# Kernel tuning notes

Hardware: AMD Instinct MI355X
Metric: run time of the kernel (lower is better)

The kernel has to match this reference:

```python
import jax, jax.numpy as jnp
import numpy as np

NEG_SLOPE = 0.2
BN_EPS = 1e-5


def gat_conv(x, W_src, W_dst, att_src, att_dst, bias, src, dst, num_nodes):
    # PyG GATConv, heads=1, concat=True, self-loops already included in (src,dst)
    h_src = x @ W_src                      # [N, H]
    h_dst = x @ W_dst                      # [N, H]
    a_src = h_src @ att_src                # [N]
    a_dst = h_dst @ att_dst                # [N]
    e = jax.nn.leaky_relu(a_src[src] + a_dst[dst], NEG_SLOPE)   # [E]
    # segment softmax over incoming edges of each dst node
    m = jax.ops.segment_max(e, dst, num_segments=num_nodes)     # [N]
    p = jnp.exp(e - m[dst])
    denom = jax.ops.segment_sum(p, dst, num_segments=num_nodes) # [N]
    alpha = p / denom[dst]                                      # [E]
    msgs = alpha[:, None] * h_src[src]                           # [E, H]
    out = jax.ops.segment_sum(msgs, dst, num_segments=num_nodes)
    return out + bias


def setup_inputs() -> dict:
    key = jax.random.key(0)
    ks = jax.random.split(key, 20)
    N, D_IN, H1, H2, FC, C = 100000, 256, 128, 128, 64, 40
    E = 1600000
    inp = {}
    inp['x'] = jax.random.normal(ks[0], (N, D_IN), dtype=jnp.float32)
    inp['edge_index'] = jax.random.randint(ks[1], (2, E), 0, N, dtype=jnp.int64)
    s = 1.0 / np.sqrt(D_IN)
    inp['W1_src'] = jax.random.uniform(ks[2], (D_IN, H1), jnp.float32, -s, s)
    inp['W1_dst'] = jax.random.uniform(ks[3], (D_IN, H1), jnp.float32, -s, s)
    inp['att1_src'] = jax.random.normal(ks[4], (H1,), jnp.float32) * 0.1
    inp['att1_dst'] = jax.random.normal(ks[5], (H1,), jnp.float32) * 0.1
    inp['b1'] = jnp.zeros((H1,), jnp.float32)
    s = 1.0 / np.sqrt(H1)
    inp['W2_src'] = jax.random.uniform(ks[6], (H1, H2), jnp.float32, -s, s)
    inp['W2_dst'] = jax.random.uniform(ks[7], (H1, H2), jnp.float32, -s, s)
    inp['att2_src'] = jax.random.normal(ks[8], (H2,), jnp.float32) * 0.1
    inp['att2_dst'] = jax.random.normal(ks[9], (H2,), jnp.float32) * 0.1
    inp['b2'] = jnp.zeros((H2,), jnp.float32)
    s = 1.0 / np.sqrt(H2)
    inp['fc1_w'] = jax.random.uniform(ks[10], (H2, FC), jnp.float32, -s, s)
    inp['fc1_b'] = jax.random.uniform(ks[11], (FC,), jnp.float32, -s, s)
    inp['gamma'] = jnp.ones((FC,), jnp.float32)
    inp['beta'] = jnp.zeros((FC,), jnp.float32)
    s = 1.0 / np.sqrt(FC)
    inp['fc2_w'] = jax.random.uniform(ks[12], (FC, C), jnp.float32, -s, s)
    inp['fc2_b'] = jax.random.uniform(ks[13], (C,), jnp.float32, -s, s)
    return inp


def reference(x, edge_index, W1_src, W1_dst, att1_src, att1_dst, b1,
              W2_src, W2_dst, att2_src, att2_dst, b2,
              fc1_w, fc1_b, gamma, beta, fc2_w, fc2_b):
    N = x.shape[0]
    loops = jnp.arange(N, dtype=edge_index.dtype)
    src = jnp.concatenate([edge_index[0], loops])
    dst = jnp.concatenate([edge_index[1], loops])
    h = jax.nn.relu(gat_conv(x, W1_src, W1_dst, att1_src, att1_dst, b1, src, dst, N))
    h = jax.nn.relu(gat_conv(h, W2_src, W2_dst, att2_src, att2_dst, b2, src, dst, N))
    h = h @ fc1_w + fc1_b                   # [N, 64]
    mu = jnp.mean(h, axis=0)
    var = jnp.var(h, axis=0)
    h = (h - mu) * jax.lax.rsqrt(var + BN_EPS) * gamma + beta
    h = jax.nn.relu(h)
    h = h @ fc2_w + fc2_b                   # [N, C]
    return jax.nn.log_softmax(h, axis=-1)
```

## Files before the change

### kernel.cpp

```cpp
#include <hip/hip_runtime.h>
#include <cstddef>

#define LSLOPE 0.2f
#define BN_EPS 1e-5f

__device__ __forceinline__ float lrelu(float x) { return x > 0.f ? x : LSLOPE * x; }

using half4 = __attribute__((ext_vector_type(4))) _Float16;
using half8 = __attribute__((ext_vector_type(8))) _Float16;
using f32x4 = __attribute__((ext_vector_type(4))) float;

struct h2 { _Float16 h, l; };
__device__ __forceinline__ h2 split2h(float x) {
  h2 r;
  r.h = (_Float16)x;
  r.l = (_Float16)(x - (float)r.h);
  return r;
}

__device__ __forceinline__ unsigned short f2bf(float x) {
  unsigned u = __float_as_uint(x);
  unsigned r = (u + 0x7fffu + ((u >> 16) & 1u)) >> 16;
  return (unsigned short)r;
}
__device__ __forceinline__ float bflo(unsigned int u) { return __uint_as_float(u << 16); }
__device__ __forceinline__ float bfhi(unsigned int u) { return __uint_as_float(u & 0xffff0000u); }

__device__ __forceinline__ void bfrag_body(const float* __restrict__ B, _Float16* __restrict__ bh,
                                           _Float16* __restrict__ bl, int K, int M, int t) {
  int KB = K >> 5;
  int lane = t & 63;
  int ckb  = t >> 6;
  int c  = ckb / KB, kb = ckb % KB;
  int mr = lane & 15, quad = lane >> 4;
  int col = c * 16 + mr;
  size_t obase = (size_t)t * 8;
#pragma unroll
  for (int j = 0; j < 8; ++j) {
    int k = kb * 32 + quad * 8 + j;
    h2 s = split2h(B[(size_t)k * M + col]);
    bh[obase + j] = s.h;
    bl[obase + j] = s.l;
  }
}

__device__ __forceinline__ void matvec_body(const float* __restrict__ A, const float* __restrict__ v,
                                            float* __restrict__ out, int R, int K, int t) {
  int w = t >> 6;
  int lane = t & 63;
  if (w >= R) return;
  const float* row = A + (size_t)w * K;
  float s = 0.f;
  for (int k = lane; k < K; k += 64) s = fmaf(row[k], v[k], s);
#pragma unroll
  for (int off = 32; off; off >>= 1) s += __shfl_xor(s, off, 64);
  if (lane == 0) out[w] = s;
}

__global__ __launch_bounds__(256) void prep_k(const float* __restrict__ W1s, const float* __restrict__ W2s,
                                              const float* __restrict__ fc1w,
                                              const float* __restrict__ W1d, const float* __restrict__ att1d,
                                              const float* __restrict__ W2d, const float* __restrict__ att2d,
                                              _Float16* B1h, _Float16* B1l, _Float16* B2h, _Float16* B2l,
                                              _Float16* Bfh, _Float16* Bfl,
                                              float* wvd1, float* wvd2) {
  int b = blockIdx.x;
  int tid = threadIdx.x;
  if (b < 16)       bfrag_body(W1s, B1h, B1l, 256, 128, b * 256 + tid);
  else if (b < 24)  bfrag_body(W2s, B2h, B2l, 128, 128, (b - 16) * 256 + tid);
  else if (b < 28)  bfrag_body(fc1w, Bfh, Bfl, 128, 64, (b - 24) * 256 + tid);
  else if (b < 92)  matvec_body(W1d, att1d, wvd1, 256, 128, (b - 28) * 256 + tid);
  else              matvec_body(W2d, att2d, wvd2, 128, 128, (b - 92) * 256 + tid);
}

template<int MCOLS>
__global__ __launch_bounds__(256) void gemm3h_k(const float* __restrict__ A,
                                                const _Float16* __restrict__ Bh,
                                                const _Float16* __restrict__ Bl,
                                                float* __restrict__ Cf,
                                                unsigned short* __restrict__ Cbf,
                                                const float* __restrict__ attv,
                                                float* __restrict__ asrc,
                                                const float* __restrict__ wvd,
                                                float* __restrict__ adout,
                                                int N, int K,
                                                const float* __restrict__ bias) {
  constexpr int CT = MCOLS / 16;
  __shared__ __align__(16) _Float16 sAh[2][128 * 32];
  __shared__ __align__(16) _Float16 sAl[2][128 * 32];
  const int tid  = threadIdx.x;
  const int row0 = blockIdx.x * 128;
  const int wv   = tid >> 6;
  const int lane = tid & 63;
  const int quad = lane >> 4;
  const int mr   = lane & 15;
  const int KB   = K >> 5;

  int srow[4], skc[4], soff[4];
  bool sok[4];
#pragma unroll
  for (int cc = 0; cc < 4; ++cc) {
    int s = tid + cc * 256;
    srow[cc] = s >> 3;
    skc[cc]  = (s & 7) << 2;
    soff[cc] = srow[cc] * 32 + ((skc[cc] + srow[cc] * 8) & 31);
    sok[cc]  = (row0 + srow[cc]) < N;
  }

  f32x4 acc[2][CT];
#pragma unroll
  for (int r = 0; r < 2; ++r)
#pragma unroll
    for (int c = 0; c < CT; ++c) acc[r][c] = (f32x4){0.f, 0.f, 0.f, 0.f};
  float pad[2] = {0.f, 0.f};

  float4 pf[4];
#pragma unroll
  for (int cc = 0; cc < 4; ++cc)
    pf[cc] = sok[cc] ? *(const float4*)&A[(size_t)(row0 + srow[cc]) * K + skc[cc]]
                     : make_float4(0.f, 0.f, 0.f, 0.f);
#pragma unroll
  for (int cc = 0; cc < 4; ++cc) {
    h2 s0 = split2h(pf[cc].x), s1 = split2h(pf[cc].y), s2 = split2h(pf[cc].z), s3 = split2h(pf[cc].w);
    half4 h4, l4;
    h4[0] = s0.h; h4[1] = s1.h; h4[2] = s2.h; h4[3] = s3.h;
    l4[0] = s0.l; l4[1] = s1.l; l4[2] = s2.l; l4[3] = s3.l;
    *(half4*)&sAh[0][soff[cc]] = h4;
    *(half4*)&sAl[0][soff[cc]] = l4;
  }
  __syncthreads();

  for (int kb = 0; kb < KB; ++kb) {
    const int cur = kb & 1, nxt = cur ^ 1;
    const int kk = kb << 5;
    if (kb + 1 < KB) {
      const int kn = (kb + 1) << 5;
#pragma unroll
      for (int cc = 0; cc < 4; ++cc)
        pf[cc] = sok[cc] ? *(const float4*)&A[(size_t)(row0 + srow[cc]) * K + kn + skc[cc]]
                         : make_float4(0.f, 0.f, 0.f, 0.f);
    }

    half8 ah[2], al[2];
#pragma unroll
    for (int r = 0; r < 2; ++r) {
      int row = wv * 32 + r * 16 + mr;
      int off = row * 32 + ((quad + row) & 3) * 8;
      ah[r] = *(const half8*)&sAh[cur][off];
      al[r] = *(const half8*)&sAl[cur][off];
    }
    if (wvd) {
      const float* wp = wvd + kk + quad * 8;
#pragma unroll
      for (int r = 0; r < 2; ++r) {
        float d = 0.f;
#pragma unroll
        for (int j = 0; j < 8; ++j) {
          float av = wp[j];
          d = fmaf((float)ah[r][j], av, d);
          d = fmaf((float)al[r][j], av, d);
        }
        pad[r] += d;
      }
    }
    const _Float16* bb_h = Bh + ((size_t)kb * 64 + lane) * 8;
    const _Float16* bb_l = Bl + ((size_t)kb * 64 + lane) * 8;
    const size_t cstride = (size_t)KB * 512;
#pragma unroll
    for (int c0 = 0; c0 < CT; c0 += 4) {
      half8 bh4[4], bl4[4];
#pragma unroll
      for (int c = 0; c < 4; ++c) {
        size_t o = (size_t)(c0 + c) * cstride;
        bh4[c] = *(const half8*)&bb_h[o];
        bl4[c] = *(const half8*)&bb_l[o];
      }
#pragma unroll
      for (int r = 0; r < 2; ++r)
#pragma unroll
        for (int c = 0; c < 4; ++c) {
          f32x4 a = acc[r][c0 + c];
          a = __builtin_amdgcn_mfma_f32_16x16x32_f16(al[r], bh4[c], a, 0, 0, 0);
          a = __builtin_amdgcn_mfma_f32_16x16x32_f16(ah[r], bl4[c], a, 0, 0, 0);
          a = __builtin_amdgcn_mfma_f32_16x16x32_f16(ah[r], bh4[c], a, 0, 0, 0);
          acc[r][c0 + c] = a;
        }
    }
    if (kb + 1 < KB) {
#pragma unroll
      for (int cc = 0; cc < 4; ++cc) {
        h2 s0 = split2h(pf[cc].x), s1 = split2h(pf[cc].y), s2 = split2h(pf[cc].z), s3 = split2h(pf[cc].w);
        half4 h4, l4;
        h4[0] = s0.h; h4[1] = s1.h; h4[2] = s2.h; h4[3] = s3.h;
        l4[0] = s0.l; l4[1] = s1.l; l4[2] = s2.l; l4[3] = s3.l;
        *(half4*)&sAh[nxt][soff[cc]] = h4;
        *(half4*)&sAl[nxt][soff[cc]] = l4;
      }
    }
    __syncthreads();
  }

  float pa[2][4];
#pragma unroll
  for (int r = 0; r < 2; ++r)
#pragma unroll
    for (int q = 0; q < 4; ++q) pa[r][q] = 0.f;

#pragma unroll
  for (int r = 0; r < 2; ++r)
#pragma unroll
    for (int c = 0; c < CT; ++c) {
      float av = attv ? attv[c * 16 + mr] : 0.f;
#pragma unroll
      for (int q = 0; q < 4; ++q) {
        int grow = row0 + wv * 32 + r * 16 + quad * 4 + q;
        float val = acc[r][c][q];
        if (bias) val += bias[c * 16 + mr];
        if (grow < N) {
          int gcol = c * 16 + mr;
          if (Cf)  Cf[(size_t)grow * MCOLS + gcol] = val;
          if (Cbf) Cbf[(size_t)grow * 128 + gcol] = f2bf(val);
        }
        if (attv) pa[r][q] = fmaf(val, av, pa[r][q]);
      }
    }
  if (attv) {
#pragma unroll
    for (int r = 0; r < 2; ++r)
#pragma unroll
      for (int q = 0; q < 4; ++q) {
        float p2 = pa[r][q];
        p2 += __shfl_xor(p2, 1, 64);
        p2 += __shfl_xor(p2, 2, 64);
        p2 += __shfl_xor(p2, 4, 64);
        p2 += __shfl_xor(p2, 8, 64);
        int grow = row0 + wv * 32 + r * 16 + quad * 4 + q;
        if (mr == 0 && grow < N) asrc[grow] = p2;
      }
  }
  if (wvd) {
#pragma unroll
    for (int r = 0; r < 2; ++r) {
      float d = pad[r];
      d += __shfl_xor(d, 16, 64);
      d += __shfl_xor(d, 32, 64);
      int grow = row0 + wv * 32 + r * 16 + mr;
      if (quad == 0 && grow < N) adout[grow] = d;
    }
  }
}

template<int MCOLS>
__global__ __launch_bounds__(256) void gemm3p_k(const _Float16* __restrict__ Ah,
                                                const _Float16* __restrict__ Al,
                                                const _Float16* __restrict__ Bh,
                                                const _Float16* __restrict__ Bl,
                                                float* __restrict__ Cf,
                                                unsigned short* __restrict__ Cbf,
                                                const float* __restrict__ attv,
                                                float* __restrict__ asrc,
                                                int N, int K,
                                                const float* __restrict__ bias) {
  constexpr int CT = MCOLS / 16;
  __shared__ __align__(16) _Float16 sAh[2][128 * 32];
  __shared__ __align__(16) _Float16 sAl[2][128 * 32];
  const int tid  = threadIdx.x;
  const int row0 = blockIdx.x * 128;
  const int wv   = tid >> 6;
  const int lane = tid & 63;
  const int quad = lane >> 4;
  const int mr   = lane & 15;
  const int KB   = K >> 5;

  int srow[2], sk8[2], soff[2];
  bool sok[2];
#pragma unroll
  for (int cc = 0; cc < 2; ++cc) {
    int s = tid + cc * 256;
    srow[cc] = s >> 2;
    sk8[cc]  = (s & 3) << 3;
    soff[cc] = srow[cc] * 32 + ((sk8[cc] + srow[cc] * 8) & 31);
    sok[cc]  = (row0 + srow[cc]) < N;
  }

  f32x4 acc[2][CT];
#pragma unroll
  for (int r = 0; r < 2; ++r)
#pragma unroll
    for (int c = 0; c < CT; ++c) acc[r][c] = (f32x4){0.f, 0.f, 0.f, 0.f};

  uint4 ph[2], pl[2];
  const uint4 z4 = make_uint4(0u, 0u, 0u, 0u);
#pragma unroll
  for (int cc = 0; cc < 2; ++cc) {
    size_t go = (size_t)(row0 + srow[cc]) * K + sk8[cc];
    ph[cc] = sok[cc] ? *(const uint4*)&Ah[go] : z4;
    pl[cc] = sok[cc] ? *(const uint4*)&Al[go] : z4;
  }
#pragma unroll
  for (int cc = 0; cc < 2; ++cc) {
    *(uint4*)&sAh[0][soff[cc]] = ph[cc];
    *(uint4*)&sAl[0][soff[cc]] = pl[cc];
  }
  __syncthreads();

  for (int kb = 0; kb < KB; ++kb) {
    const int cur = kb & 1, nxt = cur ^ 1;
    if (kb + 1 < KB) {
      const int kk = (kb + 1) << 5;
#pragma unroll
      for (int cc = 0; cc < 2; ++cc) {
        size_t go = (size_t)(row0 + srow[cc]) * K + kk + sk8[cc];
        ph[cc] = sok[cc] ? *(const uint4*)&Ah[go] : z4;
        pl[cc] = sok[cc] ? *(const uint4*)&Al[go] : z4;
      }
    }

    half8 ah[2], al[2];
#pragma unroll
    for (int r = 0; r < 2; ++r) {
      int row = wv * 32 + r * 16 + mr;
      int off = row * 32 + ((quad + row) & 3) * 8;
      ah[r] = *(const half8*)&sAh[cur][off];
      al[r] = *(const half8*)&sAl[cur][off];
    }
    const _Float16* bb_h = Bh + ((size_t)kb * 64 + lane) * 8;
    const _Float16* bb_l = Bl + ((size_t)kb * 64 + lane) * 8;
    const size_t cstride = (size_t)KB * 512;
#pragma unroll
    for (int c0 = 0; c0 < CT; c0 += 4) {
      half8 bh4[4], bl4[4];
#pragma unroll
      for (int c = 0; c < 4; ++c) {
        size_t o = (size_t)(c0 + c) * cstride;
        bh4[c] = *(const half8*)&bb_h[o];
        bl4[c] = *(const half8*)&bb_l[o];
      }
#pragma unroll
      for (int r = 0; r < 2; ++r)
#pragma unroll
        for (int c = 0; c < 4; ++c) {
          f32x4 a = acc[r][c0 + c];
          a = __builtin_amdgcn_mfma_f32_16x16x32_f16(al[r], bh4[c], a, 0, 0, 0);
          a = __builtin_amdgcn_mfma_f32_16x16x32_f16(ah[r], bl4[c], a, 0, 0, 0);
          a = __builtin_amdgcn_mfma_f32_16x16x32_f16(ah[r], bh4[c], a, 0, 0, 0);
          acc[r][c0 + c] = a;
        }
    }
    if (kb + 1 < KB) {
#pragma unroll
      for (int cc = 0; cc < 2; ++cc) {
        *(uint4*)&sAh[nxt][soff[cc]] = ph[cc];
        *(uint4*)&sAl[nxt][soff[cc]] = pl[cc];
      }
    }
    __syncthreads();
  }

  float pa[2][4];
#pragma unroll
  for (int r = 0; r < 2; ++r)
#pragma unroll
    for (int q = 0; q < 4; ++q) pa[r][q] = 0.f;

#pragma unroll
  for (int r = 0; r < 2; ++r)
#pragma unroll
    for (int c = 0; c < CT; ++c) {
      float av = attv ? attv[c * 16 + mr] : 0.f;
#pragma unroll
      for (int q = 0; q < 4; ++q) {
        int grow = row0 + wv * 32 + r * 16 + quad * 4 + q;
        float val = acc[r][c][q];
        if (bias) val += bias[c * 16 + mr];
        if (grow < N) {
          int gcol = c * 16 + mr;
          if (Cf)  Cf[(size_t)grow * MCOLS + gcol] = val;
          if (Cbf) Cbf[(size_t)grow * 128 + gcol] = f2bf(val);
        }
        if (attv) pa[r][q] = fmaf(val, av, pa[r][q]);
      }
    }
  if (attv) {
#pragma unroll
    for (int r = 0; r < 2; ++r)
#pragma unroll
      for (int q = 0; q < 4; ++q) {
        float p2 = pa[r][q];
        p2 += __shfl_xor(p2, 1, 64);
        p2 += __shfl_xor(p2, 2, 64);
        p2 += __shfl_xor(p2, 4, 64);
        p2 += __shfl_xor(p2, 8, 64);
        int grow = row0 + wv * 32 + r * 16 + quad * 4 + q;
        if (mr == 0 && grow < N) asrc[grow] = p2;
      }
  }
}

__global__ void deg_count_k(const int* __restrict__ edst, int E, int N, int* __restrict__ deg) {
  int i = blockIdx.x * 256 + threadIdx.x;
  if (i >= E + N) return;
  int d = (i < E) ? edst[i] : (i - E);
  atomicAdd(&deg[d], 1);
}

__global__ __launch_bounds__(1024) void scan1_k(const int* __restrict__ deg, int n,
                                                int* __restrict__ ex, int* __restrict__ bsum) {
  __shared__ int sm[1024];
  int t = threadIdx.x;
  int idx = blockIdx.x * 1024 + t;
  int v = (idx < n) ? deg[idx] : 0;
  sm[t] = v;
  __syncthreads();
  for (int off = 1; off < 1024; off <<= 1) {
    int tv = (t >= off) ? sm[t - off] : 0;
    __syncthreads();
    sm[t] += tv;
    __syncthreads();
  }
  if (idx < n) ex[idx] = sm[t] - v;
  if (t == 1023) bsum[blockIdx.x] = sm[t];
}

__global__ void scan3_k(int* __restrict__ ex, const int* __restrict__ bsum, int n, int nb, int total,
                        int* __restrict__ cursor) {
  __shared__ int pbase[2];
  int idx = blockIdx.x * 256 + threadIdx.x;
  int bin0 = (blockIdx.x * 256) >> 10;
  if (threadIdx.x < 2) {
    int b = bin0 + threadIdx.x;
    int s = 0;
    for (int i = 0; i < b && i < nb; ++i) s += bsum[i];
    pbase[threadIdx.x] = s;
  }
  __syncthreads();
  if (idx < n) {
    int v = ex[idx] + pbase[(idx >> 10) - bin0];
    ex[idx] = v;
    cursor[idx] = v;
  }
  if (idx == 0) ex[n] = total;
}

__global__ void scatter_range_k(const int* __restrict__ esrc, const int* __restrict__ edst,
                                int E, int N, int d0, int d1,
                                int* __restrict__ cursor, int* __restrict__ csr_src) {
  int i = blockIdx.x * 256 + threadIdx.x;
  if (i >= E + N) return;
  int d = (i < E) ? edst[i] : (i - E);
  if (d < d0 || d >= d1) return;
  int s = (i < E) ? esrc[i] : d;
  int pos = atomicAdd(&cursor[d], 1);
  csr_src[pos] = s;
}

__global__ __launch_bounds__(256) void gat_agg_k(const unsigned short* __restrict__ hbf,
                                                 const float* __restrict__ a_src,
                                                 const float* __restrict__ a_dst, const int* __restrict__ rowstart,
                                                 const int* __restrict__ csr_src, const float* __restrict__ bias,
                                                 _Float16* __restrict__ oh, _Float16* __restrict__ ol,
                                                 const float* __restrict__ wvd, float* __restrict__ ad_out,
                                                 int N) {
  int w = (blockIdx.x * blockDim.x + threadIdx.x) >> 6;
  int lane = threadIdx.x & 63;
  if (w >= N) return;
  int s0 = rowstart[w];
  int s1 = rowstart[w + 1];
  int deg = s1 - s0;
  float ad = a_dst[w];

  int sA = 0;
  float eA = -3.0e38f;
  if (lane < deg) {
    sA = csr_src[s0 + lane];
    eA = lrelu(a_src[sA] + ad);
  }
  float m = eA;
  for (int j = s0 + 64 + lane; j < s1; j += 64) {
    int s = csr_src[j];
    m = fmaxf(m, lrelu(a_src[s] + ad));
  }
#pragma unroll
  for (int off = 32; off; off >>= 1) m = fmaxf(m, __shfl_xor(m, off, 64));

  float preg = (lane < deg) ? __expf(eA - m) : 0.f;
  float den = preg;
  for (int j = s0 + 64 + lane; j < s1; j += 64) {
    int s = csr_src[j];
    den += __expf(lrelu(a_src[s] + ad) - m);
  }
#pragma unroll
  for (int off = 32; off; off >>= 1) den += __shfl_xor(den, off, 64);
  float inv = 1.f / den;

  const int q  = lane >> 4;
  const int sl = lane & 15;
  const uint4* hrow4 = (const uint4*)hbf;
  float acc[8];
#pragma unroll
  for (int i = 0; i < 8; ++i) acc[i] = 0.f;

  int lim  = deg < 64 ? deg : 64;
  int lim4 = (lim + 3) & ~3;
  for (int jj = 0; jj < lim4; jj += 4) {
    int e = jj + q;
    int s = __shfl(sA, e, 64);
    float wgt = __shfl(preg, e, 64) * inv;
    uint4 u = hrow4[(size_t)s * 16 + sl];
    acc[0] = fmaf(wgt, bflo(u.x), acc[0]);
    acc[1] = fmaf(wgt, bfhi(u.x), acc[1]);
    acc[2] = fmaf(wgt, bflo(u.y), acc[2]);
    acc[3] = fmaf(wgt, bfhi(u.y), acc[3]);
    acc[4] = fmaf(wgt, bflo(u.z), acc[4]);
    acc[5] = fmaf(wgt, bfhi(u.z), acc[5]);
    acc[6] = fmaf(wgt, bflo(u.w), acc[6]);
    acc[7] = fmaf(wgt, bfhi(u.w), acc[7]);
  }
  for (int j = s0 + 64 + q; j < s1; j += 4) {
    int s = csr_src[j];
    float wgt = __expf(lrelu(a_src[s] + ad) - m) * inv;
    uint4 u = hrow4[(size_t)s * 16 + sl];
    acc[0] = fmaf(wgt, bflo(u.x), acc[0]);
    acc[1] = fmaf(wgt, bfhi(u.x), acc[1]);
    acc[2] = fmaf(wgt, bflo(u.y), acc[2]);
    acc[3] = fmaf(wgt, bfhi(u.y), acc[3]);
    acc[4] = fmaf(wgt, bflo(u.z), acc[4]);
    acc[5] = fmaf(wgt, bfhi(u.z), acc[5]);
    acc[6] = fmaf(wgt, bflo(u.w), acc[6]);
    acc[7] = fmaf(wgt, bfhi(u.w), acc[7]);
  }
#pragma unroll
  for (int i = 0; i < 8; ++i) {
    acc[i] += __shfl_xor(acc[i], 16, 64);
    acc[i] += __shfl_xor(acc[i], 32, 64);
  }
  if (q == 0) {
    float4 b0 = *(const float4*)&bias[8 * sl];
    float4 b1 = *(const float4*)&bias[8 * sl + 4];
    float v[8];
    v[0] = fmaxf(acc[0] + b0.x, 0.f);
    v[1] = fmaxf(acc[1] + b0.y, 0.f);
    v[2] = fmaxf(acc[2] + b0.z, 0.f);
    v[3] = fmaxf(acc[3] + b0.w, 0.f);
    v[4] = fmaxf(acc[4] + b1.x, 0.f);
    v[5] = fmaxf(acc[5] + b1.y, 0.f);
    v[6] = fmaxf(acc[6] + b1.z, 0.f);
    v[7] = fmaxf(acc[7] + b1.w, 0.f);
    half8 vh, vl;
#pragma unroll
    for (int i = 0; i < 8; ++i) {
      h2 s = split2h(v[i]);
      vh[i] = s.h;
      vl[i] = s.l;
    }
    size_t base = (size_t)w * 128 + 8 * sl;
    *(half8*)&oh[base] = vh;
    *(half8*)&ol[base] = vl;
    if (wvd) {
      float4 w0 = *(const float4*)&wvd[8 * sl];
      float4 w1 = *(const float4*)&wvd[8 * sl + 4];
      float dd = v[0] * w0.x + v[1] * w0.y + v[2] * w0.z + v[3] * w0.w
               + v[4] * w1.x + v[5] * w1.y + v[6] * w1.z + v[7] * w1.w;
      dd += __shfl_xor(dd, 1, 64);
      dd += __shfl_xor(dd, 2, 64);
      dd += __shfl_xor(dd, 4, 64);
      dd += __shfl_xor(dd, 8, 64);
      if (sl == 0) ad_out[w] = dd;
    }
  }
}

__global__ __launch_bounds__(256) void bn_stats_k(const float* __restrict__ z, int N,
                                                  float* __restrict__ sums, float* __restrict__ sumsq) {
  __shared__ float ls[256], lq[256];
  int col = threadIdx.x & 63;
  int rg = threadIdx.x >> 6;
  float s = 0.f, q = 0.f;
  for (int r = blockIdx.x * 4 + rg; r < N; r += gridDim.x * 4) {
    float v = z[(size_t)r * 64 + col];
    s += v;
    q = fmaf(v, v, q);
  }
  ls[threadIdx.x] = s;
  lq[threadIdx.x] = q;
  __syncthreads();
  if (threadIdx.x < 64) {
    s = ls[col] + ls[col + 64] + ls[col + 128] + ls[col + 192];
    q = lq[col] + lq[col + 64] + lq[col + 128] + lq[col + 192];
    atomicAdd(&sums[col], s);
    atomicAdd(&sumsq[col], q);
  }
}

__global__ __launch_bounds__(256) void fc2_lsm_k(const float* __restrict__ z,
                                                 const float* __restrict__ sums, const float* __restrict__ sumsq,
                                                 const float* __restrict__ gamma, const float* __restrict__ beta,
                                                 const float* __restrict__ w,
                                                 const float* __restrict__ b, float* __restrict__ out,
                                                 int N, float invN) {
  __shared__ float ssc[64], ssh[64];
  if (threadIdx.x < 64) {
    int c = threadIdx.x;
    float mean = sums[c] * invN;
    float var = sumsq[c] * invN - mean * mean;
    float rs = rsqrtf(var + BN_EPS);
    float sc = gamma[c] * rs;
    ssc[c] = sc;
    ssh[c] = beta[c] - mean * sc;
  }
  __syncthreads();
  int n = blockIdx.x * 256 + threadIdx.x;
  if (n >= N) return;
  float o[40];
#pragma unroll
  for (int c = 0; c < 40; ++c) o[c] = b[c];
  const float* zr = z + (size_t)n * 64;
  for (int k = 0; k < 64; ++k) {
    float v = fmaxf(fmaf(zr[k], ssc[k], ssh[k]), 0.f);
#pragma unroll
    for (int c = 0; c < 40; ++c) o[c] = fmaf(v, w[k * 40 + c], o[c]);
  }
  float mx = o[0];
#pragma unroll
  for (int c = 1; c < 40; ++c) mx = fmaxf(mx, o[c]);
  float s = 0.f;
#pragma unroll
  for (int c = 0; c < 40; ++c) s += __expf(o[c] - mx);
  float ls = __logf(s);
  float* orow = out + (size_t)n * 40;
#pragma unroll
  for (int c = 0; c < 40; ++c) orow[c] = o[c] - mx - ls;
}

static inline char* al16(char* p) { return (char*)(((size_t)p + 15) & ~(size_t)15); }

extern "C" void kernel_launch(void* const* d_in, const int* in_sizes, int n_in,
                              void* d_out, int out_size, void* d_ws, size_t ws_size,
                              hipStream_t stream) {
  const float* x     = (const float*)d_in[0];
  const int*   eidx  = (const int*)d_in[1];
  const float* W1s   = (const float*)d_in[2];
  const float* W1d   = (const float*)d_in[3];
  const float* att1s = (const float*)d_in[4];
  const float* att1d = (const float*)d_in[5];
  const float* b1    = (const float*)d_in[6];
  const float* W2s   = (const float*)d_in[7];
  const float* W2d   = (const float*)d_in[8];
  const float* att2s = (const float*)d_in[9];
  const float* att2d = (const float*)d_in[10];
  const float* b2    = (const float*)d_in[11];
  const float* fc1w  = (const float*)d_in[12];
  const float* fc1b  = (const float*)d_in[13];
  const float* gamma = (const float*)d_in[14];
  const float* beta  = (const float*)d_in[15];
  const float* fc2w  = (const float*)d_in[16];
  const float* fc2b  = (const float*)d_in[17];
  float* out = (float*)d_out;

  const int N  = in_sizes[0] / 256;
  const int E  = in_sizes[1] / 2;
  const int ET = E + N;
  const int DIN = 256, H1 = 128;

  char* p = (char*)d_ws;
  int* deg      = (int*)p;     p += (size_t)N * 4;
  float* sums   = (float*)p;   p += 64 * 4;
  float* sumsq  = (float*)p;   p += 64 * 4;
  unsigned short* bhA = (unsigned short*)p; p += (size_t)N * 128 * 2;
  _Float16* hAh = (_Float16*)p;  p += (size_t)N * 128 * 2;
  _Float16* hAl = (_Float16*)p;  p += (size_t)N * 128 * 2;
  float* hF = (float*)p;         p += (size_t)N * 64 * 4;
  int* rowstart = (int*)p;     p += (size_t)(N + 1) * 4;
  int* cursor   = (int*)p;     p += (size_t)N * 4;
  int* csr_src  = (int*)p;     p += (size_t)ET * 4;
  float* a_src  = (float*)p;   p += (size_t)N * 4;
  float* a_dst  = (float*)p;   p += (size_t)N * 4;
  float* a_dst2 = (float*)p;   p += (size_t)N * 4;
  float* wvd1   = (float*)p;   p += 256 * 4;
  float* wvd2   = (float*)p;   p += 128 * 4;
  int* bsum     = (int*)p;     p += 256 * 4;
  p = al16(p);
  _Float16* B1h = (_Float16*)p; p += (size_t)256 * 128 * 2;
  _Float16* B1l = (_Float16*)p; p += (size_t)256 * 128 * 2;
  _Float16* B2h = (_Float16*)p; p += (size_t)128 * 128 * 2;
  _Float16* B2l = (_Float16*)p; p += (size_t)128 * 128 * 2;
  _Float16* Bfh = (_Float16*)p; p += (size_t)128 * 64 * 2;
  _Float16* Bfl = (_Float16*)p; p += (size_t)128 * 64 * 2;

  const int* esrc = eidx;
  const int* edst = eidx + E;

  hipMemsetAsync(deg, 0, (size_t)N * 4 + 512, stream);

  deg_count_k<<<(ET + 255) / 256, 256, 0, stream>>>(edst, E, N, deg);
  int nb = (N + 1023) / 1024;
  scan1_k<<<nb, 1024, 0, stream>>>(deg, N, rowstart, bsum);
  scan3_k<<<(N + 255) / 256, 256, 0, stream>>>(rowstart, bsum, N, nb, ET, cursor);
  {
    const int NR = 8;
    int step = (N + NR - 1) / NR;
    for (int r = 0; r < NR; ++r) {
      int d0 = r * step;
      int d1 = d0 + step < N ? d0 + step : N;
      scatter_range_k<<<(ET + 255) / 256, 256, 0, stream>>>(esrc, edst, E, N, d0, d1, cursor, csr_src);
    }
  }

  prep_k<<<124, 256, 0, stream>>>(W1s, W2s, fc1w, W1d, att1d, W2d, att2d,
                                  B1h, B1l, B2h, B2l, Bfh, Bfl, wvd1, wvd2);

  const int gemm_blocks = (N + 127) / 128;

  gemm3h_k<128><<<gemm_blocks, 256, 0, stream>>>(x, B1h, B1l, (float*)nullptr, bhA, att1s, a_src,
                                                 wvd1, a_dst, N, DIN, (const float*)nullptr);
  gat_agg_k<<<(N + 3) / 4, 256, 0, stream>>>(bhA, a_src, a_dst, rowstart, csr_src, b1,
                                             hAh, hAl, wvd2, a_dst2, N);

  gemm3p_k<128><<<gemm_blocks, 256, 0, stream>>>(hAh, hAl, B2h, B2l, (float*)nullptr, bhA, att2s, a_src,
                                                 N, H1, (const float*)nullptr);
  gat_agg_k<<<(N + 3) / 4, 256, 0, stream>>>(bhA, a_src, a_dst2, rowstart, csr_src, b2,
                                             hAh, hAl, (const float*)nullptr, (float*)nullptr, N);

  gemm3p_k<64><<<gemm_blocks, 256, 0, stream>>>(hAh, hAl, Bfh, Bfl, hF, (unsigned short*)nullptr,
                                                (const float*)nullptr, (float*)nullptr, N, H1, fc1b);
  bn_stats_k<<<512, 256, 0, stream>>>(hF, N, sums, sumsq);
  fc2_lsm_k<<<(N + 255) / 256, 256, 0, stream>>>(hF, sums, sumsq, gamma, beta, fc2w, fc2b, out,
                                                 N, 1.0f / (float)N);
}
```

Baseline: 717.7 us.

## Replace LDS-staged GEMMs with direct-load 64-row tiles split across wave pairs

Replaces the two shared-memory double-buffered GEMM kernels with one templated kernel that loads A fragments straight from global memory into registers, with no LDS and no barriers. Blocks now cover 64 rows, and the column range is split between two waves, which doubles the grid. The source attention score is now computed as a dot of the input row with a precomputed W_src·att_src vector, the same way the destination score already was, so the epilogue reduction over the output is dropped. The trade-off is that each A element is loaded by both column-half waves and reads are less coalesced, in exchange for fewer barriers and more blocks.

```diff
diff --git a/kernel.cpp b/kernel.cpp
--- a/kernel.cpp
+++ b/kernel.cpp
@@ -61,50 +61,53 @@
                                               const float* __restrict__ fc1w,
                                               const float* __restrict__ W1d, const float* __restrict__ att1d,
                                               const float* __restrict__ W2d, const float* __restrict__ att2d,
+                                              const float* __restrict__ att1s, const float* __restrict__ att2s,
                                               _Float16* B1h, _Float16* B1l, _Float16* B2h, _Float16* B2l,
                                               _Float16* Bfh, _Float16* Bfl,
-                                              float* wvd1, float* wvd2) {
+                                              float* wvd1, float* wvd2, float* wvs1, float* wvs2) {
   int b = blockIdx.x;
   int tid = threadIdx.x;
   if (b < 16)       bfrag_body(W1s, B1h, B1l, 256, 128, b * 256 + tid);
   else if (b < 24)  bfrag_body(W2s, B2h, B2l, 128, 128, (b - 16) * 256 + tid);
   else if (b < 28)  bfrag_body(fc1w, Bfh, Bfl, 128, 64, (b - 24) * 256 + tid);
   else if (b < 92)  matvec_body(W1d, att1d, wvd1, 256, 128, (b - 28) * 256 + tid);
-  else              matvec_body(W2d, att2d, wvd2, 128, 128, (b - 92) * 256 + tid);
-}
-
-template<int MCOLS>
-__global__ __launch_bounds__(256) void gemm3h_k(const float* __restrict__ A,
-                                                const _Float16* __restrict__ Bh,
-                                                const _Float16* __restrict__ Bl,
-                                                float* __restrict__ Cf,
-                                                unsigned short* __restrict__ Cbf,
-                                                const float* __restrict__ attv,
-                                                float* __restrict__ asrc,
-                                                const float* __restrict__ wvd,
-                                                float* __restrict__ adout,
-                                                int N, int K,
-                                                const float* __restrict__ bias) {
-  constexpr int CT = MCOLS / 16;
-  __shared__ __align__(16) _Float16 sAh[2][128 * 32];
-  __shared__ __align__(16) _Float16 sAl[2][128 * 32];
+  else if (b < 124) matvec_body(W2d, att2d, wvd2, 128, 128, (b - 92) * 256 + tid);
+  else if (b < 188) matvec_body(W1s, att1s, wvs1, 256, 128, (b - 124) * 256 + tid);
+  else              matvec_body(W2s, att2s, wvs2, 128, 128, (b - 188) * 256 + tid);
+}
+
+template<int K, int MCOLS, bool PS>
+__global__ __launch_bounds__(256) void gemm_dk(const float* __restrict__ Af,
+                                               const _Float16* __restrict__ Ah,
+                                               const _Float16* __restrict__ Al,
+                                               const _Float16* __restrict__ Bh,
+                                               const _Float16* __restrict__ Bl,
+                                               float* __restrict__ Cf,
+                                               unsigned short* __restrict__ Cbf,
+                                               const float* __restrict__ wvs,
+                                               float* __restrict__ asrc,
+                                               const float* __restrict__ wvd,
+                                               float* __restrict__ adout,
+                                               int N,
+                                               const float* __restrict__ bias) {
+  constexpr int KB   = K / 32;
+  constexpr int HALF = MCOLS / 2;
+  constexpr int CT   = HALF / 16;
   const int tid  = threadIdx.x;
-  const int row0 = blockIdx.x * 128;
   const int wv   = tid >> 6;
+  const int wm   = wv >> 1;
+  const int wn   = wv & 1;
   const int lane = tid & 63;
   const int quad = lane >> 4;
   const int mr   = lane & 15;
-  const int KB   = K >> 5;
-
-  int srow[4], skc[4], soff[4];
-  bool sok[4];
-#pragma unroll
-  for (int cc = 0; cc < 4; ++cc) {
-    int s = tid + cc * 256;
-    srow[cc] = s >> 3;
-    skc[cc]  = (s & 7) << 2;
-    soff[cc] = srow[cc] * 32 + ((skc[cc] + srow[cc] * 8) & 31);
-    sok[cc]  = (row0 + srow[cc]) < N;
+  const int row0 = blockIdx.x * 64;
+
+  int rowr[2];
+  bool rok[2];
+#pragma unroll
+  for (int r = 0; r < 2; ++r) {
+    rowr[r] = row0 + wm * 32 + r * 16 + mr;
+    rok[r]  = rowr[r] < N;
   }
 
   f32x4 acc[2][CT];
@@ -112,288 +115,103 @@
   for (int r = 0; r < 2; ++r)
 #pragma unroll
     for (int c = 0; c < CT; ++c) acc[r][c] = (f32x4){0.f, 0.f, 0.f, 0.f};
-  float pad[2] = {0.f, 0.f};
-
-  float4 pf[4];
-#pragma unroll
-  for (int cc = 0; cc < 4; ++cc)
-    pf[cc] = sok[cc] ? *(const float4*)&A[(size_t)(row0 + srow[cc]) * K + skc[cc]]
-                     : make_float4(0.f, 0.f, 0.f, 0.f);
-#pragma unroll
-  for (int cc = 0; cc < 4; ++cc) {
-    h2 s0 = split2h(pf[cc].x), s1 = split2h(pf[cc].y), s2 = split2h(pf[cc].z), s3 = split2h(pf[cc].w);
-    half4 h4, l4;
-    h4[0] = s0.h; h4[1] = s1.h; h4[2] = s2.h; h4[3] = s3.h;
-    l4[0] = s0.l; l4[1] = s1.l; l4[2] = s2.l; l4[3] = s3.l;
-    *(half4*)&sAh[0][soff[cc]] = h4;
-    *(half4*)&sAl[0][soff[cc]] = l4;
-  }
-  __syncthreads();
-
+  float pas[2] = {0.f, 0.f}, pad[2] = {0.f, 0.f};
+
+  const size_t cstride = (size_t)KB * 512;
+  const _Float16* bbh = Bh + (size_t)(wn * CT) * cstride + (size_t)lane * 8;
+  const _Float16* bbl = Bl + (size_t)(wn * CT) * cstride + (size_t)lane * 8;
+  const float4 zf4 = make_float4(0.f, 0.f, 0.f, 0.f);
+  const half8 hz = {(_Float16)0, (_Float16)0, (_Float16)0, (_Float16)0,
+                    (_Float16)0, (_Float16)0, (_Float16)0, (_Float16)0};
+
+#pragma unroll
   for (int kb = 0; kb < KB; ++kb) {
-    const int cur = kb & 1, nxt = cur ^ 1;
-    const int kk = kb << 5;
-    if (kb + 1 < KB) {
-      const int kn = (kb + 1) << 5;
-#pragma unroll
-      for (int cc = 0; cc < 4; ++cc)
-        pf[cc] = sok[cc] ? *(const float4*)&A[(size_t)(row0 + srow[cc]) * K + kn + skc[cc]]
-                         : make_float4(0.f, 0.f, 0.f, 0.f);
-    }
-
+    const int kk = kb * 32;
     half8 ah[2], al[2];
 #pragma unroll
     for (int r = 0; r < 2; ++r) {
-      int row = wv * 32 + r * 16 + mr;
-      int off = row * 32 + ((quad + row) & 3) * 8;
-      ah[r] = *(const half8*)&sAh[cur][off];
-      al[r] = *(const half8*)&sAl[cur][off];
-    }
-    if (wvd) {
-      const float* wp = wvd + kk + quad * 8;
+      if (PS) {
+        const size_t go = (size_t)rowr[r] * K + kk + quad * 8;
+        ah[r] = rok[r] ? *(const half8*)&Ah[go] : hz;
+        al[r] = rok[r] ? *(const half8*)&Al[go] : hz;
+      } else {
+        const float* ap = Af + (size_t)rowr[r] * K + kk + quad * 8;
+        float4 f0 = rok[r] ? *(const float4*)ap : zf4;
+        float4 f1 = rok[r] ? *(const float4*)(ap + 4) : zf4;
+        h2 s0 = split2h(f0.x), s1 = split2h(f0.y), s2 = split2h(f0.z), s3 = split2h(f0.w);
+        h2 s4 = split2h(f1.x), s5 = split2h(f1.y), s6 = split2h(f1.z), s7 = split2h(f1.w);
+        half8 h, l;
+        h[0] = s0.h; h[1] = s1.h; h[2] = s2.h; h[3] = s3.h;
+        h[4] = s4.h; h[5] = s5.h; h[6] = s6.h; h[7] = s7.h;
+        l[0] = s0.l; l[1] = s1.l; l[2] = s2.l; l[3] = s3.l;
+        l[4] = s4.l; l[5] = s5.l; l[6] = s6.l; l[7] = s7.l;
+        ah[r] = h;
+        al[r] = l;
+      }
+    }
+    if (wn == 0 && (wvs || wvd)) {
+#pragma unroll
+      for (int j = 0; j < 8; ++j) {
+        const float vs = wvs ? wvs[kk + quad * 8 + j] : 0.f;
+        const float vd = wvd ? wvd[kk + quad * 8 + j] : 0.f;
+#pragma unroll
+        for (int r = 0; r < 2; ++r) {
+          const float av = (float)ah[r][j] + (float)al[r][j];
+          if (wvs) pas[r] = fmaf(av, vs, pas[r]);
+          if (wvd) pad[r] = fmaf(av, vd, pad[r]);
+        }
+      }
+    }
+#pragma unroll
+    for (int c = 0; c < CT; ++c) {
+      const half8 bh = *(const half8*)&bbh[(size_t)kb * 512 + (size_t)c * cstride];
+      const half8 bl = *(const half8*)&bbl[(size_t)kb * 512 + (size_t)c * cstride];
 #pragma unroll
       for (int r = 0; r < 2; ++r) {
-        float d = 0.f;
-#pragma unroll
-        for (int j = 0; j < 8; ++j) {
-          float av = wp[j];
-          d = fmaf((float)ah[r][j], av, d);
-          d = fmaf((float)al[r][j], av, d);
-        }
-        pad[r] += d;
+        f32x4 a = acc[r][c];
+        a = __builtin_amdgcn_mfma_f32_16x16x32_f16(al[r], bh, a, 0, 0, 0);
+        a = __builtin_amdgcn_mfma_f32_16x16x32_f16(ah[r], bl, a, 0, 0, 0);
+        a = __builtin_amdgcn_mfma_f32_16x16x32_f16(ah[r], bh, a, 0, 0, 0);
+        acc[r][c] = a;
       }
     }
-    const _Float16* bb_h = Bh + ((size_t)kb * 64 + lane) * 8;
-    const _Float16* bb_l = Bl + ((size_t)kb * 64 + lane) * 8;
-    const size_t cstride = (size_t)KB * 512;
-#pragma unroll
-    for (int c0 = 0; c0 < CT; c0 += 4) {
-      half8 bh4[4], bl4[4];
-#pragma unroll
-      for (int c = 0; c < 4; ++c) {
-        size_t o = (size_t)(c0 + c) * cstride;
-        bh4[c] = *(const half8*)&bb_h[o];
-        bl4[c] = *(const half8*)&bb_l[o];
-      }
-#pragma unroll
-      for (int r = 0; r < 2; ++r)
-#pragma unroll
-        for (int c = 0; c < 4; ++c) {
-          f32x4 a = acc[r][c0 + c];
-          a = __builtin_amdgcn_mfma_f32_16x16x32_f16(al[r], bh4[c], a, 0, 0, 0);
-          a = __builtin_amdgcn_mfma_f32_16x16x32_f16(ah[r], bl4[c], a, 0, 0, 0);
-          a = __builtin_amdgcn_mfma_f32_16x16x32_f16(ah[r], bh4[c], a, 0, 0, 0);
-          acc[r][c0 + c] = a;
-        }
-    }
-    if (kb + 1 < KB) {
-#pragma unroll
-      for (int cc = 0; cc < 4; ++cc) {
-        h2 s0 = split2h(pf[cc].x), s1 = split2h(pf[cc].y), s2 = split2h(pf[cc].z), s3 = split2h(pf[cc].w);
-        half4 h4, l4;
-        h4[0] = s0.h; h4[1] = s1.h; h4[2] = s2.h; h4[3] = s3.h;
-        l4[0] = s0.l; l4[1] = s1.l; l4[2] = s2.l; l4[3] = s3.l;
-        *(half4*)&sAh[nxt][soff[cc]] = h4;
-        *(half4*)&sAl[nxt][soff[cc]] = l4;
-      }
-    }
-    __syncthreads();
-  }
-
-  float pa[2][4];
+  }
+
 #pragma unroll
   for (int r = 0; r < 2; ++r)
 #pragma unroll
-    for (int q = 0; q < 4; ++q) pa[r][q] = 0.f;
-
-#pragma unroll
-  for (int r = 0; r < 2; ++r)
-#pragma unroll
     for (int c = 0; c < CT; ++c) {
-      float av = attv ? attv[c * 16 + mr] : 0.f;
+      const int gcol = wn * HALF + c * 16 + mr;
+      const float bv = bias ? bias[gcol] : 0.f;
 #pragma unroll
       for (int q = 0; q < 4; ++q) {
-        int grow = row0 + wv * 32 + r * 16 + quad * 4 + q;
-        float val = acc[r][c][q];
-        if (bias) val += bias[c * 16 + mr];
+        const int grow = row0 + wm * 32 + r * 16 + quad * 4 + q;
         if (grow < N) {
-          int gcol = c * 16 + mr;
+          float val = acc[r][c][q] + bv;
           if (Cf)  Cf[(size_t)grow * MCOLS + gcol] = val;
           if (Cbf) Cbf[(size_t)grow * 128 + gcol] = f2bf(val);
         }
-        if (attv) pa[r][q] = fmaf(val, av, pa[r][q]);
       }
     }
-  if (attv) {
-#pragma unroll
-    for (int r = 0; r < 2; ++r)
-#pragma unroll
-      for (int q = 0; q < 4; ++q) {
-        float p2 = pa[r][q];
-        p2 += __shfl_xor(p2, 1, 64);
-        p2 += __shfl_xor(p2, 2, 64);
-        p2 += __shfl_xor(p2, 4, 64);
-        p2 += __shfl_xor(p2, 8, 64);
-        int grow = row0 + wv * 32 + r * 16 + quad * 4 + q;
-        if (mr == 0 && grow < N) asrc[grow] = p2;
-      }
-  }
-  if (wvd) {
+  if (wn == 0 && wvs) {
+#pragma unroll
+    for (int r = 0; r < 2; ++r) {
+      float d = pas[r];
+      d += __shfl_xor(d, 16, 64);
+      d += __shfl_xor(d, 32, 64);
+      const int grow = row0 + wm * 32 + r * 16 + mr;
+      if (quad == 0 && grow < N) asrc[grow] = d;
+    }
+  }
+  if (wn == 0 && wvd) {
 #pragma unroll
     for (int r = 0; r < 2; ++r) {
       float d = pad[r];
       d += __shfl_xor(d, 16, 64);
       d += __shfl_xor(d, 32, 64);
-      int grow = row0 + wv * 32 + r * 16 + mr;
+      const int grow = row0 + wm * 32 + r * 16 + mr;
       if (quad == 0 && grow < N) adout[grow] = d;
     }
-  }
-}
-
-template<int MCOLS>
-__global__ __launch_bounds__(256) void gemm3p_k(const _Float16* __restrict__ Ah,
-                                                const _Float16* __restrict__ Al,
-                                                const _Float16* __restrict__ Bh,
-                                                const _Float16* __restrict__ Bl,
-                                                float* __restrict__ Cf,
-                                                unsigned short* __restrict__ Cbf,
-                                                const float* __restrict__ attv,
-                                                float* __restrict__ asrc,
-                                                int N, int K,
-                                                const float* __restrict__ bias) {
-  constexpr int CT = MCOLS / 16;
-  __shared__ __align__(16) _Float16 sAh[2][128 * 32];
-  __shared__ __align__(16) _Float16 sAl[2][128 * 32];
-  const int tid  = threadIdx.x;
-  const int row0 = blockIdx.x * 128;
-  const int wv   = tid >> 6;
-  const int lane = tid & 63;
-  const int quad = lane >> 4;
-  const int mr   = lane & 15;
-  const int KB   = K >> 5;
-
-  int srow[2], sk8[2], soff[2];
-  bool sok[2];
-#pragma unroll
-  for (int cc = 0; cc < 2; ++cc) {
-    int s = tid + cc * 256;
-    srow[cc] = s >> 2;
-    sk8[cc]  = (s & 3) << 3;
-    soff[cc] = srow[cc] * 32 + ((sk8[cc] + srow[cc] * 8) & 31);
-    sok[cc]  = (row0 + srow[cc]) < N;
-  }
-
-  f32x4 acc[2][CT];
-#pragma unroll
-  for (int r = 0; r < 2; ++r)
-#pragma unroll
-    for (int c = 0; c < CT; ++c) acc[r][c] = (f32x4){0.f, 0.f, 0.f, 0.f};
-
-  uint4 ph[2], pl[2];
-  const uint4 z4 = make_uint4(0u, 0u, 0u, 0u);
-#pragma unroll
-  for (int cc = 0; cc < 2; ++cc) {
-    size_t go = (size_t)(row0 + srow[cc]) * K + sk8[cc];
-    ph[cc] = sok[cc] ? *(const uint4*)&Ah[go] : z4;
-    pl[cc] = sok[cc] ? *(const uint4*)&Al[go] : z4;
-  }
-#pragma unroll
-  for (int cc = 0; cc < 2; ++cc) {
-    *(uint4*)&sAh[0][soff[cc]] = ph[cc];
-    *(uint4*)&sAl[0][soff[cc]] = pl[cc];
-  }
-  __syncthreads();
-
-  for (int kb = 0; kb < KB; ++kb) {
-    const int cur = kb & 1, nxt = cur ^ 1;
-    if (kb + 1 < KB) {
-      const int kk = (kb + 1) << 5;
-#pragma unroll
-      for (int cc = 0; cc < 2; ++cc) {
-        size_t go = (size_t)(row0 + srow[cc]) * K + kk + sk8[cc];
-        ph[cc] = sok[cc] ? *(const uint4*)&Ah[go] : z4;
-        pl[cc] = sok[cc] ? *(const uint4*)&Al[go] : z4;
-      }
-    }
-
-    half8 ah[2], al[2];
-#pragma unroll
-    for (int r = 0; r < 2; ++r) {
-      int row = wv * 32 + r * 16 + mr;
-      int off = row * 32 + ((quad + row) & 3) * 8;
-      ah[r] = *(const half8*)&sAh[cur][off];
-      al[r] = *(const half8*)&sAl[cur][off];
-    }
-    const _Float16* bb_h = Bh + ((size_t)kb * 64 + lane) * 8;
-    const _Float16* bb_l = Bl + ((size_t)kb * 64 + lane) * 8;
-    const size_t cstride = (size_t)KB * 512;
-#pragma unroll
-    for (int c0 = 0; c0 < CT; c0 += 4) {
-      half8 bh4[4], bl4[4];
-#pragma unroll
-      for (int c = 0; c < 4; ++c) {
-        size_t o = (size_t)(c0 + c) * cstride;
-        bh4[c] = *(const half8*)&bb_h[o];
-        bl4[c] = *(const half8*)&bb_l[o];
-      }
-#pragma unroll
-      for (int r = 0; r < 2; ++r)
-#pragma unroll
-        for (int c = 0; c < 4; ++c) {
-          f32x4 a = acc[r][c0 + c];
-          a = __builtin_amdgcn_mfma_f32_16x16x32_f16(al[r], bh4[c], a, 0, 0, 0);
-          a = __builtin_amdgcn_mfma_f32_16x16x32_f16(ah[r], bl4[c], a, 0, 0, 0);
-          a = __builtin_amdgcn_mfma_f32_16x16x32_f16(ah[r], bh4[c], a, 0, 0, 0);
-          acc[r][c0 + c] = a;
-        }
-    }
-    if (kb + 1 < KB) {
-#pragma unroll
-      for (int cc = 0; cc < 2; ++cc) {
-        *(uint4*)&sAh[nxt][soff[cc]] = ph[cc];
-        *(uint4*)&sAl[nxt][soff[cc]] = pl[cc];
-      }
-    }
-    __syncthreads();
-  }
-
-  float pa[2][4];
-#pragma unroll
-  for (int r = 0; r < 2; ++r)
-#pragma unroll
-    for (int q = 0; q < 4; ++q) pa[r][q] = 0.f;
-
-#pragma unroll
-  for (int r = 0; r < 2; ++r)
-#pragma unroll
-    for (int c = 0; c < CT; ++c) {
-      float av = attv ? attv[c * 16 + mr] : 0.f;
-#pragma unroll
-      for (int q = 0; q < 4; ++q) {
-        int grow = row0 + wv * 32 + r * 16 + quad * 4 + q;
-        float val = acc[r][c][q];
-        if (bias) val += bias[c * 16 + mr];
-        if (grow < N) {
-          int gcol = c * 16 + mr;
-          if (Cf)  Cf[(size_t)grow * MCOLS + gcol] = val;
-          if (Cbf) Cbf[(size_t)grow * 128 + gcol] = f2bf(val);
-        }
-        if (attv) pa[r][q] = fmaf(val, av, pa[r][q]);
-      }
-    }
-  if (attv) {
-#pragma unroll
-    for (int r = 0; r < 2; ++r)
-#pragma unroll
-      for (int q = 0; q < 4; ++q) {
-        float p2 = pa[r][q];
-        p2 += __shfl_xor(p2, 1, 64);
-        p2 += __shfl_xor(p2, 2, 64);
-        p2 += __shfl_xor(p2, 4, 64);
-        p2 += __shfl_xor(p2, 8, 64);
-        int grow = row0 + wv * 32 + r * 16 + quad * 4 + q;
-        if (mr == 0 && grow < N) asrc[grow] = p2;
-      }
   }
 }
 
@@ -660,7 +478,6 @@
   const int N  = in_sizes[0] / 256;
   const int E  = in_sizes[1] / 2;
   const int ET = E + N;
-  const int DIN = 256, H1 = 128;
 
   char* p = (char*)d_ws;
   int* deg      = (int*)p;     p += (size_t)N * 4;
@@ -678,6 +495,8 @@
   float* a_dst2 = (float*)p;   p += (size_t)N * 4;
   float* wvd1   = (float*)p;   p += 256 * 4;
   float* wvd2   = (float*)p;   p += 128 * 4;
+  float* wvs1   = (float*)p;   p += 256 * 4;
+  float* wvs2   = (float*)p;   p += 128 * 4;
   int* bsum     = (int*)p;     p += 256 * 4;
   p = al16(p);
   _Float16* B1h = (_Float16*)p; p += (size_t)256 * 128 * 2;
@@ -706,23 +525,23 @@
     }
   }
 
-  prep_k<<<124, 256, 0, stream>>>(W1s, W2s, fc1w, W1d, att1d, W2d, att2d,
-                                  B1h, B1l, B2h, B2l, Bfh, Bfl, wvd1, wvd2);
-
-  const int gemm_blocks = (N + 127) / 128;
-
-  gemm3h_k<128><<<gemm_blocks, 256, 0, stream>>>(x, B1h, B1l, (float*)nullptr, bhA, att1s, a_src,
-                                                 wvd1, a_dst, N, DIN, (const float*)nullptr);
+  prep_k<<<220, 256, 0, stream>>>(W1s, W2s, fc1w, W1d, att1d, W2d, att2d, att1s, att2s,
+                                  B1h, B1l, B2h, B2l, Bfh, Bfl, wvd1, wvd2, wvs1, wvs2);
+
+  const int gdk = (N + 63) / 64;
+
+  gemm_dk<256, 128, false><<<gdk, 256, 0, stream>>>(x, nullptr, nullptr, B1h, B1l,
+                                                    nullptr, bhA, wvs1, a_src, wvd1, a_dst, N, nullptr);
   gat_agg_k<<<(N + 3) / 4, 256, 0, stream>>>(bhA, a_src, a_dst, rowstart, csr_src, b1,
                                              hAh, hAl, wvd2, a_dst2, N);
 
-  gemm3p_k<128><<<gemm_blocks, 256, 0, stream>>>(hAh, hAl, B2h, B2l, (float*)nullptr, bhA, att2s, a_src,
-                                                 N, H1, (const float*)nullptr);
+  gemm_dk<128, 128, true><<<gdk, 256, 0, stream>>>(nullptr, hAh, hAl, B2h, B2l,
+                                                   nullptr, bhA, wvs2, a_src, nullptr, nullptr, N, nullptr);
   gat_agg_k<<<(N + 3) / 4, 256, 0, stream>>>(bhA, a_src, a_dst2, rowstart, csr_src, b2,
-                                             hAh, hAl, (const float*)nullptr, (float*)nullptr, N);
-
-  gemm3p_k<64><<<gemm_blocks, 256, 0, stream>>>(hAh, hAl, Bfh, Bfl, hF, (unsigned short*)nullptr,
-                                                (const float*)nullptr, (float*)nullptr, N, H1, fc1b);
+                                             hAh, hAl, nullptr, nullptr, N);
+
+  gemm_dk<128, 64, true><<<gdk, 256, 0, stream>>>(nullptr, hAh, hAl, Bfh, Bfl,
+                                                  hF, nullptr, nullptr, nullptr, nullptr, nullptr, N, fc1b);
   bn_stats_k<<<512, 256, 0, stream>>>(hF, N, sums, sumsq);
   fc2_lsm_k<<<(N + 255) / 256, 256, 0, stream>>>(hF, sums, sumsq, gamma, beta, fc2w, fc2b, out,
                                                  N, 1.0f / (float)N);
```

Result: slower. 761.5 us (+6.1%).
